# Kernel tuning notes

Hardware: AMD Instinct MI355X
Metric: run time of the kernel (lower is better)

The kernel has to match this reference:

```python
import jax, jax.numpy as jnp
import numpy as np


def setup_inputs() -> dict:
    key = jax.random.key(0)
    k1, k2, k3 = jax.random.split(key, 3)
    in_features, out_features = 256, 256
    x = jax.random.normal(k1, (16, 128, in_features), dtype=jnp.float32)
    # weight[:, :, 0] = output mixing weights, weight[:, :, 1] = frequency weights
    weight = jax.random.normal(k2, (in_features, out_features, 2), dtype=jnp.float32) / np.sqrt(in_features)
    # bias[0] = output bias, bias[1:] = per-(in,out) phase
    bias = jax.random.normal(k3, (in_features + 1, out_features), dtype=jnp.float32) / np.sqrt(in_features)
    return {"x": x, "weight": weight, "bias": bias}


def reference(x, weight, bias):
    out_features = weight.shape[1]
    out_shape = x.shape[:-1] + (out_features,)
    xf = x.reshape(-1, x.shape[-1])  # [B, I]
    w_amp = weight[:, :, 0]   # [I, O]
    w_freq = weight[:, :, 1]  # [I, O]
    # bio = sin(x_bi * w_io + phase_io); out_bo = sum_i amp_io * bio
    bio = jnp.sin(jnp.einsum('bi,io->bio', xf, w_freq) + bias[1:, :])
    out = jnp.einsum('io,bio->bo', w_amp, bio) + bias[0, :]
    return out.reshape(out_shape)
```

## Files before the change

kernel.cpp:

```cpp
#include <hip/hip_runtime.h>


constexpr int IN_F   = 256;
constexpr int OUT_F  = 256;
constexpr int BROWS  = 2048;
constexpr int BTILE  = 8;
constexpr int ISPLIT = 8;
constexpr int ICHUNK = IN_F / ISPLIT;
constexpr int OPAIRS = 64;

__device__ __forceinline__ float2 pk_fma(float2 a, float2 b, float2 c) {
    return make_float2(__builtin_fmaf(a.x, b.x, c.x), __builtin_fmaf(a.y, b.y, c.y));
}
__device__ __forceinline__ float2 pk_mul(float2 a, float2 b) {
    return make_float2(a.x * b.x, a.y * b.y);
}

__global__ __launch_bounds__(OPAIRS * ISPLIT, 4) void ripple_kernel(
    const float* __restrict__ x,
    const float* __restrict__ weight,
    const float* __restrict__ bias,
    float* __restrict__ out)
{
    const int tx = threadIdx.x;
    const int g  = threadIdx.y;
    const int ob = blockIdx.x & 1;
    const int bb = blockIdx.x >> 1;
    const int b0 = bb * BTILE;
    const int oc = ob * OPAIRS + tx;

    __shared__ __align__(16) float xs_t[IN_F * BTILE];
    __shared__ float2 red[4][BTILE][OPAIRS];

    {
        const int t  = g * OPAIRS + tx;
        const int r  = t >> 6;
        const int c4 = t & 63;
        const float4 v = ((const float4*)x)[(b0 + r) * (IN_F / 4) + c4];
        xs_t[(4 * c4 + 0) * BTILE + r] = v.x;
        xs_t[(4 * c4 + 1) * BTILE + r] = v.y;
        xs_t[(4 * c4 + 2) * BTILE + r] = v.z;
        xs_t[(4 * c4 + 3) * BTILE + r] = v.w;
    }
    __syncthreads();

    float2 acc[BTILE];
#pragma unroll
    for (int r = 0; r < BTILE; ++r) acc[r] = make_float2(0.0f, 0.0f);

    const float4* __restrict__ wq  = (const float4*)weight;
    const float2* __restrict__ ph2 = (const float2*)bias;

    const float2 C7 = make_float2(-1.9841270e-4f, -1.9841270e-4f);
    const float2 C5 = make_float2( 8.3333310e-3f,  8.3333310e-3f);
    const float2 C3 = make_float2(-1.6666667e-1f, -1.6666667e-1f);
    const float2 C1 = make_float2( 1.0f, 1.0f);

    const int i0 = g * ICHUNK;
#pragma unroll 2
    for (int ii = 0; ii < ICHUNK; ++ii) {
        const int i = i0 + ii;
        const float4 w = wq[i * (OUT_F / 2) + oc];
        const float2 p = ph2[(i + 1) * (OUT_F / 2) + oc];
        const float2 amp = make_float2(w.x, w.z);
        const float2 frq = make_float2(w.y, w.w);
        const float4 xa = *(const float4*)&xs_t[i * BTILE];
        const float4 xb = *(const float4*)&xs_t[i * BTILE + 4];
        const float xv[BTILE] = {xa.x, xa.y, xa.z, xa.w, xb.x, xb.y, xb.z, xb.w};
#pragma unroll
        for (int r = 0; r < BTILE; ++r) {
            const float2 xr = make_float2(xv[r], xv[r]);
            const float2 t  = pk_fma(xr, frq, p);
            const float2 u  = pk_mul(t, t);
            float2 q        = pk_fma(C7, u, C5);
            q               = pk_fma(q,  u, C3);
            q               = pk_fma(q,  u, C1);
            const float2 s  = pk_mul(t, q);
            acc[r]          = pk_fma(amp, s, acc[r]);
        }
    }

    if (g >= 4) {
#pragma unroll
        for (int r = 0; r < BTILE; ++r) red[g - 4][r][tx] = acc[r];
    }
    __syncthreads();
    if (g < 4) {
#pragma unroll
        for (int r = 0; r < BTILE; ++r) { float2 t = red[g][r][tx]; acc[r].x += t.x; acc[r].y += t.y; }
    }
    __syncthreads();
    if (g == 2 || g == 3) {
#pragma unroll
        for (int r = 0; r < BTILE; ++r) red[g - 2][r][tx] = acc[r];
    }
    __syncthreads();
    if (g < 2) {
#pragma unroll
        for (int r = 0; r < BTILE; ++r) { float2 t = red[g][r][tx]; acc[r].x += t.x; acc[r].y += t.y; }
    }
    __syncthreads();
    if (g == 1) {
#pragma unroll
        for (int r = 0; r < BTILE; ++r) red[0][r][tx] = acc[r];
    }
    __syncthreads();
    if (g == 0) {
        const float2 bo = ph2[oc];
#pragma unroll
        for (int r = 0; r < BTILE; ++r) {
            float2 t = red[0][r][tx];
            float2 v = make_float2(acc[r].x + t.x + bo.x, acc[r].y + t.y + bo.y);
            ((float2*)out)[(b0 + r) * (OUT_F / 2) + oc] = v;
        }
    }
}

extern "C" void kernel_launch(void* const* d_in, const int* in_sizes, int n_in,
                              void* d_out, int out_size, void* d_ws, size_t ws_size,
                              hipStream_t stream) {
    const float* x      = (const float*)d_in[0];
    const float* weight = (const float*)d_in[1];
    const float* bias   = (const float*)d_in[2];
    float* out          = (float*)d_out;

    dim3 grid((BROWS / BTILE) * 2);
    dim3 block(OPAIRS, ISPLIT);
    ripple_kernel<<<grid, block, 0, stream>>>(x, weight, bias, out);
}
```

Baseline: 81.74 us.

## Retile to 16 rows per block and reduce via cross-half shuffles

Doubles the batch rows per block and the input split, narrows each block to 32 output pairs, and splits outputs four ways across the grid. Each weight and phase load is now reused across 16 rows instead of 8. The staged multi-barrier shared-memory reduction becomes one wave-level shuffle, one barrier, and a final sum by group 0. The cost is more accumulator registers per thread, which may lower occupancy under the unchanged launch bounds, plus a more serial final reduction.

```diff
diff --git a/kernel.cpp b/kernel.cpp
--- a/kernel.cpp
+++ b/kernel.cpp
@@ -4,10 +4,11 @@
 constexpr int IN_F   = 256;
 constexpr int OUT_F  = 256;
 constexpr int BROWS  = 2048;
-constexpr int BTILE  = 8;
-constexpr int ISPLIT = 8;
+constexpr int BTILE  = 16;
+constexpr int ISPLIT = 16;
 constexpr int ICHUNK = IN_F / ISPLIT;
-constexpr int OPAIRS = 64;
+constexpr int OPAIRS = 32;
+constexpr int OSPLIT = 4;
 
 __device__ __forceinline__ float2 pk_fma(float2 a, float2 b, float2 c) {
     return make_float2(__builtin_fmaf(a.x, b.x, c.x), __builtin_fmaf(a.y, b.y, c.y));
@@ -24,23 +25,26 @@
 {
     const int tx = threadIdx.x;
     const int g  = threadIdx.y;
-    const int ob = blockIdx.x & 1;
-    const int bb = blockIdx.x >> 1;
+    const int ob = blockIdx.x & (OSPLIT - 1);
+    const int bb = blockIdx.x >> 2;
     const int b0 = bb * BTILE;
     const int oc = ob * OPAIRS + tx;
 
     __shared__ __align__(16) float xs_t[IN_F * BTILE];
-    __shared__ float2 red[4][BTILE][OPAIRS];
+    __shared__ float2 red[ISPLIT / 2 - 1][BTILE][OPAIRS];
 
     {
-        const int t  = g * OPAIRS + tx;
-        const int r  = t >> 6;
-        const int c4 = t & 63;
-        const float4 v = ((const float4*)x)[(b0 + r) * (IN_F / 4) + c4];
-        xs_t[(4 * c4 + 0) * BTILE + r] = v.x;
-        xs_t[(4 * c4 + 1) * BTILE + r] = v.y;
-        xs_t[(4 * c4 + 2) * BTILE + r] = v.z;
-        xs_t[(4 * c4 + 3) * BTILE + r] = v.w;
+        const int t = g * OPAIRS + tx;
+        const int r = t & 15;
+#pragma unroll
+        for (int k = 0; k < 2; ++k) {
+            const int c4 = (t >> 4) + 32 * k;
+            const float4 v = ((const float4*)x)[(b0 + r) * (IN_F / 4) + c4];
+            xs_t[(4 * c4 + 0) * BTILE + r] = v.x;
+            xs_t[(4 * c4 + 1) * BTILE + r] = v.y;
+            xs_t[(4 * c4 + 2) * BTILE + r] = v.z;
+            xs_t[(4 * c4 + 3) * BTILE + r] = v.w;
+        }
     }
     __syncthreads();
 
@@ -64,9 +68,11 @@
         const float2 p = ph2[(i + 1) * (OUT_F / 2) + oc];
         const float2 amp = make_float2(w.x, w.z);
         const float2 frq = make_float2(w.y, w.w);
-        const float4 xa = *(const float4*)&xs_t[i * BTILE];
-        const float4 xb = *(const float4*)&xs_t[i * BTILE + 4];
-        const float xv[BTILE] = {xa.x, xa.y, xa.z, xa.w, xb.x, xb.y, xb.z, xb.w};
+        float4 xq[4];
+#pragma unroll
+        for (int q = 0; q < 4; ++q)
+            xq[q] = *(const float4*)&xs_t[i * BTILE + 4 * q];
+        const float* xv = (const float*)xq;
 #pragma unroll
         for (int r = 0; r < BTILE; ++r) {
             const float2 xr = make_float2(xv[r], xv[r]);
@@ -80,38 +86,29 @@
         }
     }
 
-    if (g >= 4) {
 #pragma unroll
-        for (int r = 0; r < BTILE; ++r) red[g - 4][r][tx] = acc[r];
+    for (int r = 0; r < BTILE; ++r) {
+        acc[r].x += __shfl_down(acc[r].x, 32);
+        acc[r].y += __shfl_down(acc[r].y, 32);
     }
-    __syncthreads();
-    if (g < 4) {
+
+    const int wv = g >> 1;
+    if ((g & 1) == 0 && wv > 0) {
 #pragma unroll
-        for (int r = 0; r < BTILE; ++r) { float2 t = red[g][r][tx]; acc[r].x += t.x; acc[r].y += t.y; }
-    }
-    __syncthreads();
-    if (g == 2 || g == 3) {
-#pragma unroll
-        for (int r = 0; r < BTILE; ++r) red[g - 2][r][tx] = acc[r];
-    }
-    __syncthreads();
-    if (g < 2) {
-#pragma unroll
-        for (int r = 0; r < BTILE; ++r) { float2 t = red[g][r][tx]; acc[r].x += t.x; acc[r].y += t.y; }
-    }
-    __syncthreads();
-    if (g == 1) {
-#pragma unroll
-        for (int r = 0; r < BTILE; ++r) red[0][r][tx] = acc[r];
+        for (int r = 0; r < BTILE; ++r) red[wv - 1][r][tx] = acc[r];
     }
     __syncthreads();
     if (g == 0) {
         const float2 bo = ph2[oc];
 #pragma unroll
         for (int r = 0; r < BTILE; ++r) {
-            float2 t = red[0][r][tx];
-            float2 v = make_float2(acc[r].x + t.x + bo.x, acc[r].y + t.y + bo.y);
-            ((float2*)out)[(b0 + r) * (OUT_F / 2) + oc] = v;
+            float s0 = acc[r].x, s1 = acc[r].y;
+#pragma unroll
+            for (int k = 0; k < ISPLIT / 2 - 1; ++k) {
+                const float2 t = red[k][r][tx];
+                s0 += t.x; s1 += t.y;
+            }
+            ((float2*)out)[(b0 + r) * (OUT_F / 2) + oc] = make_float2(s0 + bo.x, s1 + bo.y);
         }
     }
 }
@@ -124,7 +121,7 @@
     const float* bias   = (const float*)d_in[2];
     float* out          = (float*)d_out;
 
-    dim3 grid((BROWS / BTILE) * 2);
+    dim3 grid((BROWS / BTILE) * OSPLIT);
     dim3 block(OPAIRS, ISPLIT);
     ripple_kernel<<<grid, block, 0, stream>>>(x, weight, bias, out);
 }
```

Measured after the change: 89.80 us. 1.1x slower.
